# Kernel tuning notes

Measured on AMD Instinct MI355X. Metric: run time of the kernel, lower is better.

Reference implementation:

```python
import jax, jax.numpy as jnp
import numpy as np

HIDDEN, MSG, KEY, ROUNDS = 256, 64, 16, 2
LN_EPS = 1e-5


def _orthogonal(key, shape, gain):
    # mimic torch orthogonal_ init (exact values don't matter for correctness testing)
    a = jax.random.normal(key, shape, dtype=jnp.float32)
    q, r = jnp.linalg.qr(a.T if shape[0] < shape[1] else a)
    q = q * jnp.sign(jnp.diag(r))
    if shape[0] < shape[1]:
        q = q.T
    return gain * q[:shape[0], :shape[1]]


def setup_inputs() -> dict:
    key = jax.random.key(0)
    ks = jax.random.split(key, 6)
    g = float(np.sqrt(2.0))
    N = 8192
    return {
        "hidden_states": jax.random.normal(ks[0], (N, HIDDEN), dtype=jnp.float32),
        "W_msg": _orthogonal(ks[1], (MSG, HIDDEN), g),
        "b_msg": jnp.zeros((MSG,), jnp.float32),
        "W_key": _orthogonal(ks[2], (KEY, HIDDEN), g),
        "b_key": jnp.zeros((KEY,), jnp.float32),
        "W_qry": _orthogonal(ks[3], (KEY, HIDDEN), g),
        "b_qry": jnp.zeros((KEY,), jnp.float32),
        "W_agg": _orthogonal(ks[4], (HIDDEN, HIDDEN + MSG), g),
        "b_agg": jnp.zeros((HIDDEN,), jnp.float32),
        "ln_g": jnp.ones((HIDDEN,), jnp.float32),
        "ln_b": jnp.zeros((HIDDEN,), jnp.float32),
    }


def reference(hidden_states, W_msg, b_msg, W_key, b_key, W_qry, b_qry,
              W_agg, b_agg, ln_g, ln_b):
    inv_sqrt_k = 1.0 / np.sqrt(KEY)
    h = hidden_states
    attn = None
    for _ in range(ROUNDS):
        msgs = h @ W_msg.T + b_msg          # (N, MSG)
        keys = h @ W_key.T + b_key          # (N, KEY)
        qrys = h @ W_qry.T + b_qry          # (N, KEY)
        scores = (qrys @ keys.T) * inv_sqrt_k  # (N, N)
        attn = jax.nn.softmax(scores, axis=-1)
        agg_msg = attn @ msgs               # (N, MSG)
        combined = jnp.concatenate([h, agg_msg], axis=-1)  # (N, HIDDEN+MSG)
        z = combined @ W_agg.T + b_agg      # (N, HIDDEN)
        mu = jnp.mean(z, axis=-1, keepdims=True)
        var = jnp.mean(jnp.square(z - mu), axis=-1, keepdims=True)
        h = jax.nn.relu(ln_g * (z - mu) * jax.lax.rsqrt(var + LN_EPS) + ln_b)
    return h, attn
```

## Files before the change

kernel.cpp:

```cpp
#include <hip/hip_runtime.h>

constexpr int H = 256, MSGC = 64;
constexpr float LN_EPS = 1e-5f;
constexpr float QSCALE = 0.25f * 1.4426950408889634f;

typedef __attribute__((ext_vector_type(8))) short bf16x8;
typedef __attribute__((ext_vector_type(4))) float f32x4;

__device__ inline ushort f2bf(float x) {
    union { float f; unsigned u; } v; v.f = x;
    unsigned r = v.u + 0x7fffu + ((v.u >> 16) & 1u);
    return (ushort)(r >> 16);
}
__device__ inline float bf2f(ushort h) {
    union { unsigned u; float f; } v; v.u = ((unsigned)h) << 16;
    return v.f;
}
__device__ inline unsigned cvt_pk_u32(float a, float b) {
    unsigned r;
    asm("v_cvt_pk_bf16_f32 %0, %1, %2" : "=v"(r) : "v"(a), "v"(b));
    return r;
}

__global__ __launch_bounds__(256) void prep_kernel(
    const float* __restrict__ Wm, const float* __restrict__ Wk,
    const float* __restrict__ Wq, const float* __restrict__ Wa,
    ushort* __restrict__ Wph, ushort* __restrict__ Wpl,
    ushort* __restrict__ Wfh, ushort* __restrict__ Wfl)
{
    const int t = threadIdx.x, b = blockIdx.x;
    if (b < 48) {
        const int tile = b >> 3, kc = b & 7;
#pragma unroll
        for (int j2 = 0; j2 < 2; ++j2) {
            const int idx = t * 2 + j2;
            const int l = idx >> 3, e = idx & 7;
            const int col = tile * 16 + (l & 15);
            const int k = kc * 32 + (l >> 4) * 8 + e;
            float v;
            if (col < 64)      v = Wm[(size_t)col * H + k];
            else if (col < 80) v = Wk[(size_t)(col - 64) * H + k];
            else               v = QSCALE * Wq[(size_t)(col - 80) * H + k];
            ushort hi = f2bf(v);
            Wph[(size_t)b * 512 + idx] = hi;
            Wpl[(size_t)b * 512 + idx] = f2bf(v - bf2f(hi));
        }
    } else {
        const int unit = b - 48;
        const int ctg = unit / 10, kc = unit % 10;
#pragma unroll
        for (int j2 = 0; j2 < 2; ++j2) {
            const int idx = t * 2 + j2;
            const int l = idx >> 3, e = idx & 7;
            const int col = ctg * 16 + (l & 15);
            const int k = kc * 32 + (l >> 4) * 8 + e;
            const float v = Wa[(size_t)col * 320 + k];
            ushort hi = f2bf(v);
            Wfh[(size_t)unit * 512 + idx] = hi;
            Wfl[(size_t)unit * 512 + idx] = f2bf(v - bf2f(hi));
        }
    }
}

__global__ __launch_bounds__(128) void proj_kernel(
    const float* __restrict__ h,
    const ushort* __restrict__ Wph, const ushort* __restrict__ Wpl,
    const float* __restrict__ bm, const float* __restrict__ bk, const float* __restrict__ bq,
    ushort* __restrict__ msgsF, ushort* __restrict__ kh, ushort* __restrict__ kl,
    ushort* __restrict__ qh, ushort* __restrict__ ql, int n)
{
    constexpr int AST = 264;
    __shared__ ushort Ahi[16 * AST];
    __shared__ ushort Alo[16 * AST];
    const int t = threadIdx.x, lane = t & 63, w = t >> 6;
    const int gq = lane >> 4, c = lane & 15;
    const int r0 = blockIdx.x * 16;
    const float4* hsrc = (const float4*)(h + (size_t)r0 * H);
#pragma unroll
    for (int u = 0; u < 8; ++u) {
        const int idx = t + 128 * u;
        const int row = idx >> 6, c4 = idx & 63;
        float4 v = hsrc[idx];
        ushort4 hi, lo;
        hi.x = f2bf(v.x); lo.x = f2bf(v.x - bf2f(hi.x));
        hi.y = f2bf(v.y); lo.y = f2bf(v.y - bf2f(hi.y));
        hi.z = f2bf(v.z); lo.z = f2bf(v.z - bf2f(hi.z));
        hi.w = f2bf(v.w); lo.w = f2bf(v.w - bf2f(hi.w));
        *(ushort4*)&Ahi[row * AST + c4 * 4] = hi;
        *(ushort4*)&Alo[row * AST + c4 * 4] = lo;
    }
    __syncthreads();
    f32x4 acc[3] = {{0,0,0,0},{0,0,0,0},{0,0,0,0}};
    for (int kc = 0; kc < 8; ++kc) {
        const bf16x8 afh = *(const bf16x8*)&Ahi[c * AST + kc * 32 + gq * 8];
        const bf16x8 afl = *(const bf16x8*)&Alo[c * AST + kc * 32 + gq * 8];
#pragma unroll
        for (int ct = 0; ct < 3; ++ct) {
            const int unit = (w * 3 + ct) * 8 + kc;
            const bf16x8 whi = *(const bf16x8*)(Wph + (size_t)unit * 512 + lane * 8);
            const bf16x8 wlo = *(const bf16x8*)(Wpl + (size_t)unit * 512 + lane * 8);
            acc[ct] = __builtin_amdgcn_mfma_f32_16x16x32_bf16(afh, whi, acc[ct], 0, 0, 0);
            acc[ct] = __builtin_amdgcn_mfma_f32_16x16x32_bf16(afh, wlo, acc[ct], 0, 0, 0);
            acc[ct] = __builtin_amdgcn_mfma_f32_16x16x32_bf16(afl, whi, acc[ct], 0, 0, 0);
        }
    }
#pragma unroll
    for (int ct = 0; ct < 3; ++ct) {
        const int tile = w * 3 + ct;
        if (tile < 4) {
            const float bb = bm[tile * 16 + c];
#pragma unroll
            for (int r = 0; r < 4; ++r) {
                const int j = r0 + gq * 4 + r;
                const int o = j & 31;
                const int lam = ((o & 15) << 1) | (o >> 4);
                const size_t idx = ((size_t)(j >> 5) * 4 + tile) * 512
                                 + (lam >> 3) * 128 + c * 8 + (lam & 7);
                msgsF[idx] = f2bf(acc[ct][r] + bb);
            }
        } else if (tile == 4) {
            const float bb = bk[c];
#pragma unroll
            for (int r = 0; r < 4; ++r) {
                const int j = r0 + gq * 4 + r;
                const float v = acc[ct][r] + bb;
                const ushort hi = f2bf(v);
                kh[(size_t)j * 16 + c] = hi;
                kl[(size_t)j * 16 + c] = f2bf(v - bf2f(hi));
            }
        } else {
            const float bb = QSCALE * bq[c];
#pragma unroll
            for (int r = 0; r < 4; ++r) {
                const int j = r0 + gq * 4 + r;
                const float v = acc[ct][r] + bb;
                const ushort hi = f2bf(v);
                qh[(size_t)j * 16 + c] = hi;
                ql[(size_t)j * 16 + c] = f2bf(v - bf2f(hi));
            }
        }
    }
}

__device__ __forceinline__ void loadK(bf16x8* dst, const ushort* __restrict__ kh,
                                      int j0, int g, int c) {
#pragma unroll
    for (int js = 0; js < 4; ++js)
        dst[js] = *(const bf16x8*)(kh + (size_t)(j0 + js * 16 + c) * 16 + 8 * (g & 1));
}

__device__ __forceinline__ void qk_tile(const bf16x8* b1s, const ushort* __restrict__ kl,
                                        int j0, int g, int c, bf16x8 a1, bf16x8 a2,
                                        const bf16x8 zer, f32x4* pd) {
    const f32x4 z4 = {0.f, 0.f, 0.f, 0.f};
    bf16x8 b2s[4];
#pragma unroll
    for (int js = 0; js < 4; ++js)
        b2s[js] = (g < 2) ? *(const bf16x8*)(kl + (size_t)(j0 + js * 16 + c) * 16 + 8 * g) : zer;
#pragma unroll
    for (int js = 0; js < 4; ++js) {
        pd[js] = __builtin_amdgcn_mfma_f32_16x16x32_bf16(a1, b1s[js], z4, 0, 0, 0);
        pd[js] = __builtin_amdgcn_mfma_f32_16x16x32_bf16(a2, b2s[js], pd[js], 0, 0, 0);
    }
}

__device__ __forceinline__ void expstore_bf(const f32x4* pd, ushort* Pbuf, float* l,
                                            int w, int g, int c) {
#pragma unroll
    for (int r = 0; r < 4; ++r) {
        const int row = w * 16 + g * 4 + r;
        const float e0 = exp2f(pd[0][r]);
        const float e1 = exp2f(pd[1][r]);
        const float e2 = exp2f(pd[2][r]);
        const float e3 = exp2f(pd[3][r]);
        l[r] += (e0 + e1) + (e2 + e3);
        ushort* base = Pbuf + row * 64;
        *(unsigned*)&base[(((c >> 2)) ^ (row & 7)) * 8 + (c & 3) * 2]     = cvt_pk_u32(e0, e1);
        *(unsigned*)&base[((4 + (c >> 2)) ^ (row & 7)) * 8 + (c & 3) * 2] = cvt_pk_u32(e2, e3);
    }
}
__device__ __forceinline__ void expstore_n_bf(const f32x4* pd, ushort* Pbuf, const float* rinv,
                                              int w, int g, int c) {
#pragma unroll
    for (int r = 0; r < 4; ++r) {
        const int row = w * 16 + g * 4 + r;
        const float e0 = exp2f(pd[0][r]) * rinv[r];
        const float e1 = exp2f(pd[1][r]) * rinv[r];
        const float e2 = exp2f(pd[2][r]) * rinv[r];
        const float e3 = exp2f(pd[3][r]) * rinv[r];
        ushort* base = Pbuf + row * 64;
        *(unsigned*)&base[(((c >> 2)) ^ (row & 7)) * 8 + (c & 3) * 2]     = cvt_pk_u32(e0, e1);
        *(unsigned*)&base[((4 + (c >> 2)) ^ (row & 7)) * 8 + (c & 3) * 2] = cvt_pk_u32(e2, e3);
    }
}

__device__ __forceinline__ void pv_bf(const ushort* __restrict__ Pbuf,
                                      const ushort* __restrict__ msgsF,
                                      int j0, int g, int c, int w, int lane, f32x4* accv) {
    const int arow = w * 16 + c;
    const int sw = arow & 7;
#pragma unroll
    for (int gam = 0; gam < 2; ++gam) {
        const bf16x8 af = *(const bf16x8*)&Pbuf[arow * 64 + ((gam * 4 + g) ^ sw) * 8];
        const size_t mbase = ((size_t)(j0 >> 5) + gam) * 4;
#pragma unroll
        for (int mt = 0; mt < 4; ++mt) {
            bf16x8 bfr = *((const bf16x8*)(msgsF + (mbase + mt) * 512) + lane);
            accv[mt] = __builtin_amdgcn_mfma_f32_16x16x32_bf16(af, bfr, accv[mt], 0, 0, 0);
        }
    }
}

__device__ __forceinline__ void attn_write_bf(const ushort* __restrict__ Pbuf,
                                              float* __restrict__ attn,
                                              int i0, int j0, int n, int lane, int w) {
    const int g4 = lane >> 4, c4 = lane & 15;
#pragma unroll
    for (int u = 0; u < 4; ++u) {
        const int row = w * 16 + u * 4 + g4;
        const int sw = row & 7;
        const ushort* base = Pbuf + row * 64;
        float* arow = attn + (size_t)(i0 + row) * n + j0;
#pragma unroll
        for (int gam = 0; gam < 2; ++gam) {
            const unsigned uv = *(const unsigned*)&base[((gam * 4 + (c4 >> 2)) ^ sw) * 8 + (c4 & 3) * 2];
            arow[gam * 32 + c4]      = bf2f((ushort)(uv & 0xffffu));
            arow[gam * 32 + c4 + 16] = bf2f((ushort)(uv >> 16));
        }
    }
}

__global__ __launch_bounds__(256, 4) void flash1_kernel(
    const ushort* __restrict__ qh, const ushort* __restrict__ ql,
    const ushort* __restrict__ kh, const ushort* __restrict__ kl,
    const ushort* __restrict__ msgsF,
    float* __restrict__ aggO, float* __restrict__ aggL, int n)
{
    __shared__ ushort P0[64 * 64];
    __shared__ ushort P1[64 * 64];
    const int t = threadIdx.x, lane = t & 63, w = t >> 6;
    const int g = lane >> 4, c = lane & 15;
    const int i0 = blockIdx.x * 64;
    bf16x8 zer = {0,0,0,0,0,0,0,0};
    f32x4 z4 = {0.f, 0.f, 0.f, 0.f};
    const ushort* qsrc = (g < 2) ? qh : ql;
    bf16x8 a1 = *(const bf16x8*)(qsrc + (size_t)(i0 + w * 16 + c) * 16 + 8 * (g & 1));
    bf16x8 a2 = (g < 2) ? a1 : zer;
    float l[4] = {0.f, 0.f, 0.f, 0.f};
    f32x4 accv[4] = {z4, z4, z4, z4};
    const int nj = n / 8, jb = blockIdx.y * nj;
    bf16x8 bA[4], bB[4];
    loadK(bA, kh, jb, g, c);
    loadK(bB, kh, jb + 64, g, c);
    {
        f32x4 pd[4];
        qk_tile(bA, kl, jb, g, c, a1, a2, zer, pd);
        expstore_bf(pd, P0, l, w, g, c);
    }
    loadK(bA, kh, jb + 128, g, c);
    {
        f32x4 pd[4];
        qk_tile(bB, kl, jb + 64, g, c, a1, a2, zer, pd);
        pv_bf(P0, msgsF, jb, g, c, w, lane, accv);
        expstore_bf(pd, P1, l, w, g, c);
    }
    for (int p = 1; p < 8; ++p) {
        const int tA = jb + p * 128, tB = tA + 64;
        loadK(bB, kh, tB, g, c);
        {
            f32x4 pd[4];
            qk_tile(bA, kl, tA, g, c, a1, a2, zer, pd);
            pv_bf(P1, msgsF, tA - 64, g, c, w, lane, accv);
            expstore_bf(pd, P0, l, w, g, c);
        }
        loadK(bA, kh, (p < 7) ? tA + 128 : tB, g, c);
        {
            f32x4 pd[4];
            qk_tile(bB, kl, tB, g, c, a1, a2, zer, pd);
            pv_bf(P0, msgsF, tA, g, c, w, lane, accv);
            expstore_bf(pd, P1, l, w, g, c);
        }
    }
    pv_bf(P1, msgsF, jb + nj - 64, g, c, w, lane, accv);
#pragma unroll
    for (int r = 0; r < 4; ++r)
#pragma unroll
        for (int d2 = 1; d2 < 16; d2 <<= 1) l[r] += __shfl_xor(l[r], d2, 64);
#pragma unroll
    for (int mt = 0; mt < 4; ++mt)
#pragma unroll
        for (int r = 0; r < 4; ++r)
            aggO[((size_t)blockIdx.y * n + i0 + w * 16 + g * 4 + r) * MSGC + mt * 16 + c] = accv[mt][r];
    if (c == 0) {
#pragma unroll
        for (int r = 0; r < 4; ++r)
            aggL[(size_t)blockIdx.y * n + i0 + w * 16 + g * 4 + r] = l[r];
    }
}

__global__ __launch_bounds__(256, 4) void stats_kernel(
    const ushort* __restrict__ qh, const ushort* __restrict__ ql,
    const ushort* __restrict__ kh, const ushort* __restrict__ kl,
    float* __restrict__ rowl_p, int n)
{
    const int t = threadIdx.x, lane = t & 63, w = t >> 6;
    const int g = lane >> 4, c = lane & 15;
    const int iq = blockIdx.x * 64 + w * 16 + c;
    bf16x8 zer = {0,0,0,0,0,0,0,0};
    const ushort* qsrc = (g < 2) ? qh : ql;
    bf16x8 a1 = *(const bf16x8*)(qsrc + (size_t)iq * 16 + 8 * (g & 1));
    bf16x8 a2 = (g < 2) ? a1 : zer;
    const int nj = n / 8, jb = blockIdx.y * nj;
    float l[4] = {0.f, 0.f, 0.f, 0.f};
    bf16x8 bA[4], bB[4];
    loadK(bA, kh, jb, g, c);
    for (int p = 0; p < 8; ++p) {
        const int t0 = jb + p * 128, t1 = t0 + 64;
        const int t2 = (p < 7) ? t0 + 128 : t1;
        loadK(bB, kh, t1, g, c);
        {
            f32x4 pd[4];
            qk_tile(bA, kl, t0, g, c, a1, a2, zer, pd);
#pragma unroll
            for (int js = 0; js < 4; ++js)
#pragma unroll
                for (int r = 0; r < 4; ++r) l[r] += exp2f(pd[js][r]);
        }
        loadK(bA, kh, t2, g, c);
        {
            f32x4 pd[4];
            qk_tile(bB, kl, t1, g, c, a1, a2, zer, pd);
#pragma unroll
            for (int js = 0; js < 4; ++js)
#pragma unroll
                for (int r = 0; r < 4; ++r) l[r] += exp2f(pd[js][r]);
        }
    }
#pragma unroll
    for (int r = 0; r < 4; ++r)
#pragma unroll
        for (int d2 = 1; d2 < 16; d2 <<= 1) l[r] += __shfl_xor(l[r], d2, 64);
    if (c == 0) {
        const int q0 = blockIdx.x * 64 + w * 16 + g * 4;
#pragma unroll
        for (int r = 0; r < 4; ++r)
            rowl_p[(size_t)blockIdx.y * n + q0 + r] = l[r];
    }
}

__global__ __launch_bounds__(256, 4) void pass2_kernel(
    const ushort* __restrict__ qh, const ushort* __restrict__ ql,
    const ushort* __restrict__ kh, const ushort* __restrict__ kl,
    const ushort* __restrict__ msgsF, const float* __restrict__ rowl_p,
    float* __restrict__ aggO, float* __restrict__ attn, int n)
{
    __shared__ ushort P0[64 * 64];
    __shared__ ushort P1[64 * 64];
    const int t = threadIdx.x, lane = t & 63, w = t >> 6;
    const int g = lane >> 4, c = lane & 15;
    const int i0 = blockIdx.x * 64;
    bf16x8 zer = {0,0,0,0,0,0,0,0};
    f32x4 z4 = {0.f, 0.f, 0.f, 0.f};
    const ushort* qsrc = (g < 2) ? qh : ql;
    bf16x8 a1 = *(const bf16x8*)(qsrc + (size_t)(i0 + w * 16 + c) * 16 + 8 * (g & 1));
    bf16x8 a2 = (g < 2) ? a1 : zer;
    float rinv[4];
#pragma unroll
    for (int r = 0; r < 4; ++r) {
        const int q = i0 + w * 16 + g * 4 + r;
        float L = 0.f;
#pragma unroll
        for (int p = 0; p < 8; ++p) L += rowl_p[(size_t)p * n + q];
        rinv[r] = 1.f / L;
    }
    f32x4 accv[4] = {z4, z4, z4, z4};
    const int nj = n / 8, jb = blockIdx.y * nj;
    bf16x8 bA[4], bB[4];
    loadK(bA, kh, jb, g, c);
    loadK(bB, kh, jb + 64, g, c);
    {
        f32x4 pd[4];
        qk_tile(bA, kl, jb, g, c, a1, a2, zer, pd);
        expstore_n_bf(pd, P0, rinv, w, g, c);
    }
    loadK(bA, kh, jb + 128, g, c);
    {
        f32x4 pd[4];
        qk_tile(bB, kl, jb + 64, g, c, a1, a2, zer, pd);
        pv_bf(P0, msgsF, jb, g, c, w, lane, accv);
        attn_write_bf(P0, attn, i0, jb, n, lane, w);
        expstore_n_bf(pd, P1, rinv, w, g, c);
    }
    for (int p = 1; p < 8; ++p) {
        const int tA = jb + p * 128, tB = tA + 64;
        loadK(bB, kh, tB, g, c);
        {
            f32x4 pd[4];
            qk_tile(bA, kl, tA, g, c, a1, a2, zer, pd);
            pv_bf(P1, msgsF, tA - 64, g, c, w, lane, accv);
            attn_write_bf(P1, attn, i0, tA - 64, n, lane, w);
            expstore_n_bf(pd, P0, rinv, w, g, c);
        }
        loadK(bA, kh, (p < 7) ? tA + 128 : tB, g, c);
        {
            f32x4 pd[4];
            qk_tile(bB, kl, tB, g, c, a1, a2, zer, pd);
            pv_bf(P0, msgsF, tA, g, c, w, lane, accv);
            attn_write_bf(P0, attn, i0, tA, n, lane, w);
            expstore_n_bf(pd, P1, rinv, w, g, c);
        }
    }
    pv_bf(P1, msgsF, jb + nj - 64, g, c, w, lane, accv);
    attn_write_bf(P1, attn, i0, jb + nj - 64, n, lane, w);
#pragma unroll
    for (int mt = 0; mt < 4; ++mt)
#pragma unroll
        for (int r = 0; r < 4; ++r) {
            const int row = w * 16 + g * 4 + r;
            aggO[((size_t)blockIdx.y * n + i0 + row) * MSGC + mt * 16 + c] = accv[mt][r];
        }
}

template <bool FLASH>
__global__ __launch_bounds__(256) void aggln_kernel(
    const float* __restrict__ h, const float* __restrict__ aggO,
    const float* __restrict__ aggL,
    const ushort* __restrict__ Wfh, const ushort* __restrict__ Wfl,
    const float* __restrict__ ba,
    const float* __restrict__ gg, const float* __restrict__ bb,
    float* __restrict__ hout, int n)
{
    constexpr int AST = 328;
    __shared__ ushort Ahi[16 * AST];
    __shared__ ushort Alo[16 * AST];
    __shared__ float Linv[16];
    __shared__ float red1[16][4], red2[16][4];
    const int t = threadIdx.x, lane = t & 63, w = t >> 6;
    const int gq = lane >> 4, c = lane & 15;
    const int r0 = blockIdx.x * 16;
    const float4* hsrc = (const float4*)(h + (size_t)r0 * H);
#pragma unroll
    for (int u = 0; u < 4; ++u) {
        const int idx = t + 256 * u;
        const int row = idx >> 6, c4 = idx & 63;
        float4 v = hsrc[idx];
        ushort4 hi, lo;
        hi.x = f2bf(v.x); lo.x = f2bf(v.x - bf2f(hi.x));
        hi.y = f2bf(v.y); lo.y = f2bf(v.y - bf2f(hi.y));
        hi.z = f2bf(v.z); lo.z = f2bf(v.z - bf2f(hi.z));
        hi.w = f2bf(v.w); lo.w = f2bf(v.w - bf2f(hi.w));
        *(ushort4*)&Ahi[row * AST + c4 * 4] = hi;
        *(ushort4*)&Alo[row * AST + c4 * 4] = lo;
    }
    if (FLASH && t < 16) {
        float L = 0.f;
#pragma unroll
        for (int p = 0; p < 8; ++p) L += aggL[(size_t)p * n + r0 + t];
        Linv[t] = 1.f / L;
    }
    __syncthreads();
    {
        const int row = t >> 4, c4 = t & 15;
        float4 s = {0.f, 0.f, 0.f, 0.f};
#pragma unroll
        for (int p = 0; p < 8; ++p) {
            const float4 v = *(const float4*)(aggO + (size_t)p * n * MSGC
                               + (size_t)(r0 + row) * MSGC + c4 * 4);
            s.x += v.x; s.y += v.y; s.z += v.z; s.w += v.w;
        }
        if (FLASH) { const float li = Linv[row]; s.x *= li; s.y *= li; s.z *= li; s.w *= li; }
        ushort4 hi, lo;
        hi.x = f2bf(s.x); lo.x = f2bf(s.x - bf2f(hi.x));
        hi.y = f2bf(s.y); lo.y = f2bf(s.y - bf2f(hi.y));
        hi.z = f2bf(s.z); lo.z = f2bf(s.z - bf2f(hi.z));
        hi.w = f2bf(s.w); lo.w = f2bf(s.w - bf2f(hi.w));
        *(ushort4*)&Ahi[row * AST + 256 + c4 * 4] = hi;
        *(ushort4*)&Alo[row * AST + 256 + c4 * 4] = lo;
    }
    __syncthreads();
    f32x4 acc[4] = {{0,0,0,0},{0,0,0,0},{0,0,0,0},{0,0,0,0}};
    for (int kc = 0; kc < 10; ++kc) {
        const bf16x8 afh = *(const bf16x8*)&Ahi[c * AST + kc * 32 + gq * 8];
        const bf16x8 afl = *(const bf16x8*)&Alo[c * AST + kc * 32 + gq * 8];
#pragma unroll
        for (int ct = 0; ct < 4; ++ct) {
            const int ctg = w * 4 + ct;
            const bf16x8 whi = *(const bf16x8*)(Wfh + ((size_t)(ctg * 10 + kc)) * 512 + lane * 8);
            const bf16x8 wlo = *(const bf16x8*)(Wfl + ((size_t)(ctg * 10 + kc)) * 512 + lane * 8);
            acc[ct] = __builtin_amdgcn_mfma_f32_16x16x32_bf16(afh, whi, acc[ct], 0, 0, 0);
            acc[ct] = __builtin_amdgcn_mfma_f32_16x16x32_bf16(afh, wlo, acc[ct], 0, 0, 0);
            acc[ct] = __builtin_amdgcn_mfma_f32_16x16x32_bf16(afl, whi, acc[ct], 0, 0, 0);
        }
    }
    float bav[4], gv[4], bv[4];
#pragma unroll
    for (int ct = 0; ct < 4; ++ct) {
        const int col = w * 64 + ct * 16 + c;
        bav[ct] = ba[col]; gv[ct] = gg[col]; bv[ct] = bb[col];
    }
#pragma unroll
    for (int ct = 0; ct < 4; ++ct) {
        acc[ct][0] += bav[ct]; acc[ct][1] += bav[ct];
        acc[ct][2] += bav[ct]; acc[ct][3] += bav[ct];
    }
#pragma unroll
    for (int r = 0; r < 4; ++r) {
        float s1 = 0.f, s2 = 0.f;
#pragma unroll
        for (int ct = 0; ct < 4; ++ct) { const float v = acc[ct][r]; s1 += v; s2 += v * v; }
#pragma unroll
        for (int d = 1; d < 16; d <<= 1) { s1 += __shfl_xor(s1, d, 64); s2 += __shfl_xor(s2, d, 64); }
        if (c == 0) { red1[gq * 4 + r][w] = s1; red2[gq * 4 + r][w] = s2; }
    }
    __syncthreads();
#pragma unroll
    for (int r = 0; r < 4; ++r) {
        const int row = gq * 4 + r;
        const float s1 = red1[row][0] + red1[row][1] + red1[row][2] + red1[row][3];
        const float s2 = red2[row][0] + red2[row][1] + red2[row][2] + red2[row][3];
        const float mu = s1 * (1.f / 256.f);
        const float var = s2 * (1.f / 256.f) - mu * mu;
        const float rs = rsqrtf(var + LN_EPS);
#pragma unroll
        for (int ct = 0; ct < 4; ++ct) {
            float o = (acc[ct][r] - mu) * rs * gv[ct] + bv[ct];
            hout[(size_t)(r0 + row) * H + w * 64 + ct * 16 + c] = fmaxf(o, 0.f);
        }
    }
}

extern "C" void kernel_launch(void* const* d_in, const int* in_sizes, int n_in,
                              void* d_out, int out_size, void* d_ws, size_t ws_size,
                              hipStream_t stream)
{
    const float* hs = (const float*)d_in[0];
    const float* Wm = (const float*)d_in[1];
    const float* bm = (const float*)d_in[2];
    const float* Wk = (const float*)d_in[3];
    const float* bk = (const float*)d_in[4];
    const float* Wq = (const float*)d_in[5];
    const float* bq = (const float*)d_in[6];
    const float* Wa = (const float*)d_in[7];
    const float* ba = (const float*)d_in[8];
    const float* lg = (const float*)d_in[9];
    const float* lb = (const float*)d_in[10];
    const int n = in_sizes[0] / H;

    char* wp = (char*)d_ws;
    auto alloc = [&](size_t bytes) { void* p = (void*)wp; wp += (bytes + 255) & ~(size_t)255; return p; };
    float*  h2     = (float*)alloc((size_t)n * H * 4);
    ushort* qh     = (ushort*)alloc((size_t)n * 16 * 2);
    ushort* ql     = (ushort*)alloc((size_t)n * 16 * 2);
    ushort* kh     = (ushort*)alloc((size_t)n * 16 * 2);
    ushort* kl     = (ushort*)alloc((size_t)n * 16 * 2);
    ushort* msgsF  = (ushort*)alloc((size_t)MSGC * n * 2);
    float*  rowl_p = (float*)alloc((size_t)8 * n * 4);
    float*  aggO   = (float*)alloc((size_t)8 * n * MSGC * 4);
    float*  aggL   = (float*)alloc((size_t)8 * n * 4);
    ushort* Wph    = (ushort*)alloc((size_t)48 * 512 * 2);
    ushort* Wpl    = (ushort*)alloc((size_t)48 * 512 * 2);
    ushort* Wfh    = (ushort*)alloc((size_t)160 * 512 * 2);
    ushort* Wfl    = (ushort*)alloc((size_t)160 * 512 * 2);

    float* hOut = (float*)d_out;
    float* attn = hOut + (size_t)n * H;

    prep_kernel<<<208, 256, 0, stream>>>(Wm, Wk, Wq, Wa, Wph, Wpl, Wfh, Wfl);

    proj_kernel<<<n / 16, 128, 0, stream>>>(hs, Wph, Wpl, bm, bk, bq, msgsF, kh, kl, qh, ql, n);
    flash1_kernel<<<dim3(n / 64, 8), 256, 0, stream>>>(qh, ql, kh, kl, msgsF,
                                                       aggO, aggL, n);
    aggln_kernel<true><<<n / 16, 256, 0, stream>>>(hs, aggO, aggL, Wfh, Wfl,
                                                   ba, lg, lb, h2, n);
    proj_kernel<<<n / 16, 128, 0, stream>>>(h2, Wph, Wpl, bm, bk, bq, msgsF, kh, kl, qh, ql, n);
    stats_kernel<<<dim3(n / 64, 8), 256, 0, stream>>>(qh, ql, kh, kl, rowl_p, n);
    pass2_kernel<<<dim3(n / 64, 8), 256, 0, stream>>>(qh, ql, kh, kl, msgsF,
                                                      rowl_p, aggO, attn, n);
    aggln_kernel<false><<<n / 16, 256, 0, stream>>>(h2, aggO, aggL, Wfh, Wfl,
                                                    ba, lg, lb, hOut, n);
}
```

Before: 255.8 us.

## Store pass-2 probabilities as fp32 in LDS and write attention with float4 stores

In the second-round pass, the normalized probabilities are now kept as fp32 in shared memory with an XOR swizzle. The attention output is written from there with one 16-byte store per lane, and the values are packed to bf16 only when building the PV MFMA operand. A second, naturally ordered copy of the message matrix is written by the projection kernel so that pass2 can read the PV operand with the new layout. This is meant to cut the scattered 4-byte attention stores and the bf16 round-trip on attention values, at the cost of double the LDS, which can lower occupancy, and an extra message buffer write.

```diff
diff --git a/kernel.cpp b/kernel.cpp
--- a/kernel.cpp
+++ b/kernel.cpp
@@ -20,6 +20,14 @@
     unsigned r;
     asm("v_cvt_pk_bf16_f32 %0, %1, %2" : "=v"(r) : "v"(a), "v"(b));
     return r;
+}
+__device__ inline bf16x8 pack_bf16x8(float4 f0, float4 f1) {
+    union { unsigned u[4]; bf16x8 v; } cv;
+    cv.u[0] = cvt_pk_u32(f0.x, f0.y);
+    cv.u[1] = cvt_pk_u32(f0.z, f0.w);
+    cv.u[2] = cvt_pk_u32(f1.x, f1.y);
+    cv.u[3] = cvt_pk_u32(f1.z, f1.w);
+    return cv.v;
 }
 
 __global__ __launch_bounds__(256) void prep_kernel(
@@ -66,7 +74,8 @@
     const float* __restrict__ h,
     const ushort* __restrict__ Wph, const ushort* __restrict__ Wpl,
     const float* __restrict__ bm, const float* __restrict__ bk, const float* __restrict__ bq,
-    ushort* __restrict__ msgsF, ushort* __restrict__ kh, ushort* __restrict__ kl,
+    ushort* __restrict__ msgsFn, ushort* __restrict__ msgsFp,
+    ushort* __restrict__ kh, ushort* __restrict__ kl,
     ushort* __restrict__ qh, ushort* __restrict__ ql, int n)
 {
     constexpr int AST = 264;
@@ -113,10 +122,11 @@
             for (int r = 0; r < 4; ++r) {
                 const int j = r0 + gq * 4 + r;
                 const int o = j & 31;
+                const ushort mv = f2bf(acc[ct][r] + bb);
+                const size_t base = ((size_t)(j >> 5) * 4 + tile) * 512 + c * 8;
+                msgsFn[base + ((o >> 3) & 3) * 128 + (o & 7)] = mv;
                 const int lam = ((o & 15) << 1) | (o >> 4);
-                const size_t idx = ((size_t)(j >> 5) * 4 + tile) * 512
-                                 + (lam >> 3) * 128 + c * 8 + (lam & 7);
-                msgsF[idx] = f2bf(acc[ct][r] + bb);
+                msgsFp[base + (lam >> 3) * 128 + (lam & 7)] = mv;
             }
         } else if (tile == 4) {
             const float bb = bk[c];
@@ -179,23 +189,9 @@
         *(unsigned*)&base[((4 + (c >> 2)) ^ (row & 7)) * 8 + (c & 3) * 2] = cvt_pk_u32(e2, e3);
     }
 }
-__device__ __forceinline__ void expstore_n_bf(const f32x4* pd, ushort* Pbuf, const float* rinv,
-                                              int w, int g, int c) {
-#pragma unroll
-    for (int r = 0; r < 4; ++r) {
-        const int row = w * 16 + g * 4 + r;
-        const float e0 = exp2f(pd[0][r]) * rinv[r];
-        const float e1 = exp2f(pd[1][r]) * rinv[r];
-        const float e2 = exp2f(pd[2][r]) * rinv[r];
-        const float e3 = exp2f(pd[3][r]) * rinv[r];
-        ushort* base = Pbuf + row * 64;
-        *(unsigned*)&base[(((c >> 2)) ^ (row & 7)) * 8 + (c & 3) * 2]     = cvt_pk_u32(e0, e1);
-        *(unsigned*)&base[((4 + (c >> 2)) ^ (row & 7)) * 8 + (c & 3) * 2] = cvt_pk_u32(e2, e3);
-    }
-}
 
 __device__ __forceinline__ void pv_bf(const ushort* __restrict__ Pbuf,
-                                      const ushort* __restrict__ msgsF,
+                                      const ushort* __restrict__ msgsFp,
                                       int j0, int g, int c, int w, int lane, f32x4* accv) {
     const int arow = w * 16 + c;
     const int sw = arow & 7;
@@ -205,35 +201,61 @@
         const size_t mbase = ((size_t)(j0 >> 5) + gam) * 4;
 #pragma unroll
         for (int mt = 0; mt < 4; ++mt) {
-            bf16x8 bfr = *((const bf16x8*)(msgsF + (mbase + mt) * 512) + lane);
+            bf16x8 bfr = *((const bf16x8*)(msgsFp + (mbase + mt) * 512) + lane);
             accv[mt] = __builtin_amdgcn_mfma_f32_16x16x32_bf16(af, bfr, accv[mt], 0, 0, 0);
         }
     }
 }
 
-__device__ __forceinline__ void attn_write_bf(const ushort* __restrict__ Pbuf,
-                                              float* __restrict__ attn,
-                                              int i0, int j0, int n, int lane, int w) {
-    const int g4 = lane >> 4, c4 = lane & 15;
+__device__ __forceinline__ void expstore_n_f32(const f32x4* pd, float* Pbuf, const float* rinv,
+                                               int w, int g, int c) {
+#pragma unroll
+    for (int js = 0; js < 4; ++js)
+#pragma unroll
+        for (int r = 0; r < 4; ++r) {
+            const int row = w * 16 + g * 4 + r;
+            const float pp = exp2f(pd[js][r]) * rinv[r];
+            Pbuf[row * 64 + ((js * 16 + c) ^ ((row & 7) << 2))] = pp;
+        }
+}
+
+__device__ __forceinline__ void pv_f32(const float* __restrict__ P,
+                                       const ushort* __restrict__ msgsFn,
+                                       int j0, int g, int c, int w, int lane, f32x4* accv) {
+#pragma unroll
+    for (int ks = 0; ks < 2; ++ks) {
+        const int arow = w * 16 + c;
+        const int sw = (arow & 7) << 2;
+        const int colb = ks * 32 + 8 * g;
+        float4 f0 = *(const float4*)&P[arow * 64 + ((colb) ^ sw)];
+        float4 f1 = *(const float4*)&P[arow * 64 + ((colb + 4) ^ sw)];
+        bf16x8 af = pack_bf16x8(f0, f1);
+        const size_t mbase = ((size_t)(j0 >> 5) + ks) * 4;
+#pragma unroll
+        for (int mt = 0; mt < 4; ++mt) {
+            bf16x8 bfr = *((const bf16x8*)(msgsFn + (mbase + mt) * 512) + lane);
+            accv[mt] = __builtin_amdgcn_mfma_f32_16x16x32_bf16(af, bfr, accv[mt], 0, 0, 0);
+        }
+    }
+}
+
+__device__ __forceinline__ void attn_write4(const float* __restrict__ Pbuf,
+                                            float* __restrict__ attn,
+                                            int i0, int j0, int n, int lane, int w) {
+    const int c4 = lane & 15;
 #pragma unroll
     for (int u = 0; u < 4; ++u) {
-        const int row = w * 16 + u * 4 + g4;
-        const int sw = row & 7;
-        const ushort* base = Pbuf + row * 64;
-        float* arow = attn + (size_t)(i0 + row) * n + j0;
-#pragma unroll
-        for (int gam = 0; gam < 2; ++gam) {
-            const unsigned uv = *(const unsigned*)&base[((gam * 4 + (c4 >> 2)) ^ sw) * 8 + (c4 & 3) * 2];
-            arow[gam * 32 + c4]      = bf2f((ushort)(uv & 0xffffu));
-            arow[gam * 32 + c4 + 16] = bf2f((ushort)(uv >> 16));
-        }
+        const int row = w * 16 + u * 4 + (lane >> 4);
+        const int sw = (row & 7) << 2;
+        float4 v = *(const float4*)&Pbuf[row * 64 + ((c4 * 4) ^ sw)];
+        *(float4*)(attn + (size_t)(i0 + row) * n + j0 + c4 * 4) = v;
     }
 }
 
 __global__ __launch_bounds__(256, 4) void flash1_kernel(
     const ushort* __restrict__ qh, const ushort* __restrict__ ql,
     const ushort* __restrict__ kh, const ushort* __restrict__ kl,
-    const ushort* __restrict__ msgsF,
+    const ushort* __restrict__ msgsFp,
     float* __restrict__ aggO, float* __restrict__ aggL, int n)
 {
     __shared__ ushort P0[64 * 64];
@@ -261,7 +283,7 @@
     {
         f32x4 pd[4];
         qk_tile(bB, kl, jb + 64, g, c, a1, a2, zer, pd);
-        pv_bf(P0, msgsF, jb, g, c, w, lane, accv);
+        pv_bf(P0, msgsFp, jb, g, c, w, lane, accv);
         expstore_bf(pd, P1, l, w, g, c);
     }
     for (int p = 1; p < 8; ++p) {
@@ -270,18 +292,18 @@
         {
             f32x4 pd[4];
             qk_tile(bA, kl, tA, g, c, a1, a2, zer, pd);
-            pv_bf(P1, msgsF, tA - 64, g, c, w, lane, accv);
+            pv_bf(P1, msgsFp, tA - 64, g, c, w, lane, accv);
             expstore_bf(pd, P0, l, w, g, c);
         }
         loadK(bA, kh, (p < 7) ? tA + 128 : tB, g, c);
         {
             f32x4 pd[4];
             qk_tile(bB, kl, tB, g, c, a1, a2, zer, pd);
-            pv_bf(P0, msgsF, tA, g, c, w, lane, accv);
+            pv_bf(P0, msgsFp, tA, g, c, w, lane, accv);
             expstore_bf(pd, P1, l, w, g, c);
         }
     }
-    pv_bf(P1, msgsF, jb + nj - 64, g, c, w, lane, accv);
+    pv_bf(P1, msgsFp, jb + nj - 64, g, c, w, lane, accv);
 #pragma unroll
     for (int r = 0; r < 4; ++r)
 #pragma unroll
@@ -351,11 +373,11 @@
 __global__ __launch_bounds__(256, 4) void pass2_kernel(
     const ushort* __restrict__ qh, const ushort* __restrict__ ql,
     const ushort* __restrict__ kh, const ushort* __restrict__ kl,
-    const ushort* __restrict__ msgsF, const float* __restrict__ rowl_p,
+    const ushort* __restrict__ msgsFn, const float* __restrict__ rowl_p,
     float* __restrict__ aggO, float* __restrict__ attn, int n)
 {
-    __shared__ ushort P0[64 * 64];
-    __shared__ ushort P1[64 * 64];
+    __shared__ float P0[64 * 64];
+    __shared__ float P1[64 * 64];
     const int t = threadIdx.x, lane = t & 63, w = t >> 6;
     const int g = lane >> 4, c = lane & 15;
     const int i0 = blockIdx.x * 64;
@@ -381,15 +403,15 @@
     {
         f32x4 pd[4];
         qk_tile(bA, kl, jb, g, c, a1, a2, zer, pd);
-        expstore_n_bf(pd, P0, rinv, w, g, c);
+        expstore_n_f32(pd, P0, rinv, w, g, c);
     }
     loadK(bA, kh, jb + 128, g, c);
     {
         f32x4 pd[4];
         qk_tile(bB, kl, jb + 64, g, c, a1, a2, zer, pd);
-        pv_bf(P0, msgsF, jb, g, c, w, lane, accv);
-        attn_write_bf(P0, attn, i0, jb, n, lane, w);
-        expstore_n_bf(pd, P1, rinv, w, g, c);
+        attn_write4(P0, attn, i0, jb, n, lane, w);
+        pv_f32(P0, msgsFn, jb, g, c, w, lane, accv);
+        expstore_n_f32(pd, P1, rinv, w, g, c);
     }
     for (int p = 1; p < 8; ++p) {
         const int tA = jb + p * 128, tB = tA + 64;
@@ -397,21 +419,21 @@
         {
             f32x4 pd[4];
             qk_tile(bA, kl, tA, g, c, a1, a2, zer, pd);
-            pv_bf(P1, msgsF, tA - 64, g, c, w, lane, accv);
-            attn_write_bf(P1, attn, i0, tA - 64, n, lane, w);
-            expstore_n_bf(pd, P0, rinv, w, g, c);
+            attn_write4(P1, attn, i0, tA - 64, n, lane, w);
+            pv_f32(P1, msgsFn, tA - 64, g, c, w, lane, accv);
+            expstore_n_f32(pd, P0, rinv, w, g, c);
         }
         loadK(bA, kh, (p < 7) ? tA + 128 : tB, g, c);
         {
             f32x4 pd[4];
             qk_tile(bB, kl, tB, g, c, a1, a2, zer, pd);
-            pv_bf(P0, msgsF, tA, g, c, w, lane, accv);
-            attn_write_bf(P0, attn, i0, tA, n, lane, w);
-            expstore_n_bf(pd, P1, rinv, w, g, c);
-        }
-    }
-    pv_bf(P1, msgsF, jb + nj - 64, g, c, w, lane, accv);
-    attn_write_bf(P1, attn, i0, jb + nj - 64, n, lane, w);
+            attn_write4(P0, attn, i0, tA, n, lane, w);
+            pv_f32(P0, msgsFn, tA, g, c, w, lane, accv);
+            expstore_n_f32(pd, P1, rinv, w, g, c);
+        }
+    }
+    attn_write4(P1, attn, i0, jb + nj - 64, n, lane, w);
+    pv_f32(P1, msgsFn, jb + nj - 64, g, c, w, lane, accv);
 #pragma unroll
     for (int mt = 0; mt < 4; ++mt)
 #pragma unroll
@@ -553,7 +575,8 @@
     ushort* ql     = (ushort*)alloc((size_t)n * 16 * 2);
     ushort* kh     = (ushort*)alloc((size_t)n * 16 * 2);
     ushort* kl     = (ushort*)alloc((size_t)n * 16 * 2);
-    ushort* msgsF  = (ushort*)alloc((size_t)MSGC * n * 2);
+    ushort* msgsFn = (ushort*)alloc((size_t)MSGC * n * 2);
+    ushort* msgsFp = (ushort*)alloc((size_t)MSGC * n * 2);
     float*  rowl_p = (float*)alloc((size_t)8 * n * 4);
     float*  aggO   = (float*)alloc((size_t)8 * n * MSGC * 4);
     float*  aggL   = (float*)alloc((size_t)8 * n * 4);
@@ -567,14 +590,16 @@
 
     prep_kernel<<<208, 256, 0, stream>>>(Wm, Wk, Wq, Wa, Wph, Wpl, Wfh, Wfl);
 
-    proj_kernel<<<n / 16, 128, 0, stream>>>(hs, Wph, Wpl, bm, bk, bq, msgsF, kh, kl, qh, ql, n);
-    flash1_kernel<<<dim3(n / 64, 8), 256, 0, stream>>>(qh, ql, kh, kl, msgsF,
+    proj_kernel<<<n / 16, 128, 0, stream>>>(hs, Wph, Wpl, bm, bk, bq,
+                                            msgsFn, msgsFp, kh, kl, qh, ql, n);
+    flash1_kernel<<<dim3(n / 64, 8), 256, 0, stream>>>(qh, ql, kh, kl, msgsFp,
                                                        aggO, aggL, n);
     aggln_kernel<true><<<n / 16, 256, 0, stream>>>(hs, aggO, aggL, Wfh, Wfl,
                                                    ba, lg, lb, h2, n);
-    proj_kernel<<<n / 16, 128, 0, stream>>>(h2, Wph, Wpl, bm, bk, bq, msgsF, kh, kl, qh, ql, n);
+    proj_kernel<<<n / 16, 128, 0, stream>>>(h2, Wph, Wpl, bm, bk, bq,
+                                            msgsFn, msgsFp, kh, kl, qh, ql, n);
     stats_kernel<<<dim3(n / 64, 8), 256, 0, stream>>>(qh, ql, kh, kl, rowl_p, n);
-    pass2_kernel<<<dim3(n / 64, 8), 256, 0, stream>>>(qh, ql, kh, kl, msgsF,
+    pass2_kernel<<<dim3(n / 64, 8), 256, 0, stream>>>(qh, ql, kh, kl, msgsFn,
                                                       rowl_p, aggO, attn, n);
     aggln_kernel<false><<<n / 16, 256, 0, stream>>>(h2, aggO, aggL, Wfh, Wfl,
                                                     ba, lg, lb, hOut, n);
```

Measured after the change: 247.1 us. -3.4%, faster.
